# Kernel optimization log

Measured on AMD Instinct MI355X. Metric: run time of the kernel, lower is better.

## Reference

```python
import jax, jax.numpy as jnp
import numpy as np


def gcn_conv(x, src, dst, W, b, num_nodes):
    # PyG GCNConv with add_self_loops=True, symmetric normalization.
    # src/dst already include self-loops.
    ones = jnp.ones(src.shape[0], dtype=x.dtype)
    deg = jax.ops.segment_sum(ones, dst, num_segments=num_nodes)  # [N]
    dinv = jnp.where(deg > 0, jax.lax.rsqrt(deg), 0.0)
    norm = dinv[src] * dinv[dst]                                   # [E+N]
    h = x @ W                                                      # [N, out]
    msg = h[src] * norm[:, None]                                   # gather + scale
    out = jax.ops.segment_sum(msg, dst, num_segments=num_nodes)    # scatter-add
    return out + b


def setup_inputs() -> dict:
    key = jax.random.key(0)
    k1, k2, k3, k4 = jax.random.split(key, 4)
    N, E = 50000, 1600000
    IN, HID, OUT = 1536, 256, 128
    x = jax.random.normal(k1, (N, IN), dtype=jnp.float32)
    edge_index = jax.random.randint(k2, (2, E), 0, N, dtype=jnp.int64)
    # Glorot-style scaled weights
    W1 = jax.random.normal(k3, (IN, HID), dtype=jnp.float32) / np.sqrt(IN)
    W2 = jax.random.normal(k4, (HID, OUT), dtype=jnp.float32) / np.sqrt(HID)
    b1 = jnp.zeros((HID,), dtype=jnp.float32)
    b2 = jnp.zeros((OUT,), dtype=jnp.float32)
    return {"x": x, "edge_index": edge_index, "W1": W1, "b1": b1,
            "W2": W2, "b2": b2, "num_nodes": N}


def reference(x, edge_index, W1, b1, W2, b2, num_nodes):
    loop = jnp.arange(num_nodes, dtype=edge_index.dtype)
    src = jnp.concatenate([edge_index[0], loop])
    dst = jnp.concatenate([edge_index[1], loop])
    h = gcn_conv(x, src, dst, W1, b1, num_nodes)
    h = jax.nn.relu(h)
    h = gcn_conv(h, src, dst, W2, b2, num_nodes)
    # F.normalize(h, dim=1): x / max(||x||_2, 1e-12)
    nrm = jnp.linalg.norm(h, axis=1, keepdims=True)
    return h / jnp.maximum(nrm, 1e-12)
```

## Files before the change

kernel.cpp:

```cpp
#include <hip/hip_runtime.h>

typedef __attribute__((ext_vector_type(4))) float f32x4;
typedef __attribute__((ext_vector_type(2))) float f32x2;
typedef __attribute__((ext_vector_type(8))) short s16x8;
typedef __attribute__((ext_vector_type(4))) unsigned short u16x4;
typedef __attribute__((ext_vector_type(2))) unsigned short u16x2;

static __device__ __forceinline__ unsigned short f2bf(float f) {
  unsigned int u = __builtin_bit_cast(unsigned int, f);
  u += 0x7fffu + ((u >> 16) & 1u);
  return (unsigned short)(u >> 16);
}
static __device__ __forceinline__ float bf2f(unsigned short h) {
  unsigned int u = ((unsigned int)h) << 16;
  return __builtin_bit_cast(float, u);
}

__global__ void zero_k(int* p, int n) {
  int i = blockIdx.x * 256 + threadIdx.x;
  if (i < n) p[i] = 0;
}
__global__ void deg_count_k(const int* __restrict__ edges, int* cnt, int E) {
  int e = blockIdx.x * 256 + threadIdx.x;
  if (e < E) atomicAdd(&cnt[edges[E + e]], 1);
}
__global__ void dinv_k(const int* __restrict__ cnt, float* dinv, int N) {
  int i = blockIdx.x * 256 + threadIdx.x;
  if (i < N) dinv[i] = rsqrtf((float)(cnt[i] + 1));
}

__global__ __launch_bounds__(256) void scan1_k(const int* __restrict__ cnt,
                                               int* __restrict__ loc,
                                               int* __restrict__ bsum, int N) {
  int t = threadIdx.x;
  int i0 = blockIdx.x * 1024 + t * 4;
  int c[4];
#pragma unroll
  for (int j = 0; j < 4; ++j) c[j] = (i0 + j < N) ? cnt[i0 + j] : 0;
  int tsum = c[0] + c[1] + c[2] + c[3];
  int lane = t & 63, wv = t >> 6;
  int incl = tsum;
#pragma unroll
  for (int off = 1; off < 64; off <<= 1) {
    int u = __shfl_up(incl, off, 64);
    if (lane >= off) incl += u;
  }
  __shared__ int ws[4];
  if (lane == 63) ws[wv] = incl;
  __syncthreads();
  int wbase = 0;
  for (int w = 0; w < wv; ++w) wbase += ws[w];
  int run = wbase + incl - tsum;
#pragma unroll
  for (int j = 0; j < 4; ++j) {
    if (i0 + j < N) loc[i0 + j] = run;
    run += c[j];
  }
  if (t == 255) bsum[blockIdx.x] = wbase + incl;
}
__global__ void scan2_k(int* bsum, int nb) {
  int lane = threadIdx.x;
  int v = (lane < nb) ? bsum[lane] : 0;
  int incl = v;
#pragma unroll
  for (int off = 1; off < 64; off <<= 1) {
    int u = __shfl_up(incl, off, 64);
    if (lane >= off) incl += u;
  }
  if (lane < nb) bsum[lane] = incl - v;
}
__global__ void addoff_k(int* loc, const int* __restrict__ bsum, int N) {
  int i = blockIdx.x * 256 + threadIdx.x;
  if (i < N) loc[i] += bsum[i >> 10];
}
__global__ void fill_k(const int* __restrict__ edges, const int* __restrict__ row,
                       int* cursor, int* __restrict__ csr, int E) {
  int e = blockIdx.x * 256 + threadIdx.x;
  if (e < E) {
    int s = edges[e], d = edges[E + e];
    int pos = atomicAdd(&cursor[d], 1);
    csr[row[d] + pos] = s;
  }
}

__global__ void convw_k(const float* __restrict__ W, unsigned short* __restrict__ Wt, int K, int Nn) {
  int t = blockIdx.x * 256 + threadIdx.x;
  if (t < K * Nn) {
    int n = t / K;
    int k = t - n * K;
    Wt[n * K + k] = f2bf(W[(long long)k * Nn + n]);
  }
}

template <int KTOT, int NTOT, bool A_BF16>
__global__ __launch_bounds__(256, 2) void gemm_k(
    const void* __restrict__ Aptr, const unsigned short* __restrict__ Bt,
    const float* __restrict__ dinv, unsigned short* __restrict__ outg, int M) {
  constexpr int BM = 128, BK = 32, LD = BK + 8;
  constexpr int STRIP = NTOT / 4;
  constexpr int NF = STRIP / 16;
  constexpr int CH = NTOT / 64;

  __shared__ unsigned short Asm_[BM * LD];
  __shared__ unsigned short Bsm_[NTOT * LD];

  const int tid = threadIdx.x;
  const int wave = tid >> 6;
  const int lane = tid & 63;
  const int fr = lane & 15;
  const int quad = lane >> 4;
  const int m0 = blockIdx.x * BM;

  f32x4 acc[8][NF];
#pragma unroll
  for (int i = 0; i < 8; ++i)
#pragma unroll
    for (int j = 0; j < NF; ++j) { f32x4 z = {0.f, 0.f, 0.f, 0.f}; acc[i][j] = z; }

  const int sr = tid >> 1;
  const int sc = (tid & 1) << 4;
  const bool arow_ok = (m0 + sr) < M;
  const float* arowf = (const float*)Aptr + (long long)(m0 + sr) * KTOT;
  const unsigned short* arowh = (const unsigned short*)Aptr + (long long)(m0 + sr) * KTOT;

  float va[16];
  s16x8 vah[2];

  auto loadA = [&](int k0) {
    if constexpr (A_BF16) {
      if (arow_ok) {
        vah[0] = *(const s16x8*)(arowh + k0 + sc);
        vah[1] = *(const s16x8*)(arowh + k0 + sc + 8);
      } else {
        s16x8 z = {0, 0, 0, 0, 0, 0, 0, 0};
        vah[0] = z; vah[1] = z;
      }
    } else {
      if (arow_ok) {
        const f32x4* p = (const f32x4*)(arowf + k0 + sc);
        f32x4 v0 = p[0], v1 = p[1], v2 = p[2], v3 = p[3];
#pragma unroll
        for (int j = 0; j < 4; ++j) { va[j] = v0[j]; va[4 + j] = v1[j]; va[8 + j] = v2[j]; va[12 + j] = v3[j]; }
      } else {
#pragma unroll
        for (int j = 0; j < 16; ++j) va[j] = 0.0f;
      }
    }
  };
  s16x8 vb[CH];
  auto loadB = [&](int k0) {
#pragma unroll
    for (int c = 0; c < CH; ++c) {
      int ch = tid + c * 256;
      int br = ch >> 2;
      int bc = (ch & 3) << 3;
      vb[c] = *(const s16x8*)&Bt[(long long)br * KTOT + k0 + bc];
    }
  };

  loadA(0);
  loadB(0);

  for (int k0 = 0; k0 < KTOT; k0 += BK) {
    s16x8 h0, h1;
    if constexpr (A_BF16) {
      h0 = vah[0]; h1 = vah[1];
    } else {
#pragma unroll
      for (int j = 0; j < 8; ++j) { h0[j] = (short)f2bf(va[j]); h1[j] = (short)f2bf(va[8 + j]); }
    }
    s16x8 vbc[CH];
#pragma unroll
    for (int c = 0; c < CH; ++c) vbc[c] = vb[c];

    __syncthreads();
    *(s16x8*)&Asm_[sr * LD + sc] = h0;
    *(s16x8*)&Asm_[sr * LD + sc + 8] = h1;
#pragma unroll
    for (int c = 0; c < CH; ++c) {
      int ch = tid + c * 256;
      int br = ch >> 2;
      int bc = (ch & 3) << 3;
      *(s16x8*)&Bsm_[br * LD + bc] = vbc[c];
    }
    __syncthreads();

    if (k0 + BK < KTOT) { loadA(k0 + BK); loadB(k0 + BK); }

    s16x8 af[8], bfr[NF];
#pragma unroll
    for (int mi = 0; mi < 8; ++mi) af[mi] = *(const s16x8*)&Asm_[(mi * 16 + fr) * LD + quad * 8];
#pragma unroll
    for (int ni = 0; ni < NF; ++ni) bfr[ni] = *(const s16x8*)&Bsm_[(wave * STRIP + ni * 16 + fr) * LD + quad * 8];
#pragma unroll
    for (int mi = 0; mi < 8; ++mi)
#pragma unroll
      for (int ni = 0; ni < NF; ++ni)
        acc[mi][ni] = __builtin_amdgcn_mfma_f32_16x16x32_bf16(af[mi], bfr[ni], acc[mi][ni], 0, 0, 0);
  }

#pragma unroll
  for (int mi = 0; mi < 8; ++mi) {
    int mbase = mi * 16 + quad * 4;
#pragma unroll
    for (int r = 0; r < 4; ++r) {
      int gm = m0 + mbase + r;
      if (gm < M) {
        float dv = dinv[gm];
#pragma unroll
        for (int ni = 0; ni < NF; ++ni) {
          int col = wave * STRIP + ni * 16 + fr;
          outg[(long long)gm * NTOT + col] = f2bf(acc[mi][ni][r] * dv);
        }
      }
    }
  }
}

__global__ __launch_bounds__(256) void agg1_k(const int* __restrict__ csr,
                                              const int* __restrict__ row,
                                              const int* __restrict__ cnt,
                                              const unsigned short* __restrict__ g,
                                              const float* __restrict__ bias,
                                              const float* __restrict__ dinv,
                                              unsigned short* __restrict__ h, int N) {
  int node = blockIdx.x * 4 + (threadIdx.x >> 6);
  if (node >= N) return;
  int lane = threadIdx.x & 63;
  int f0 = lane << 2;
  u16x4 sv = *(const u16x4*)&g[(long long)node * 256 + f0];
  f32x4 s = {bf2f(sv[0]), bf2f(sv[1]), bf2f(sv[2]), bf2f(sv[3])};
  int start = row[node], len = cnt[node];
  int j = 0;
  for (; j + 8 <= len; j += 8) {
    int idx[8];
#pragma unroll
    for (int t = 0; t < 8; ++t) idx[t] = csr[start + j + t];
    u16x4 v[8];
#pragma unroll
    for (int t = 0; t < 8; ++t) v[t] = *(const u16x4*)&g[(long long)idx[t] * 256 + f0];
#pragma unroll
    for (int t = 0; t < 8; ++t) {
      s[0] += bf2f(v[t][0]); s[1] += bf2f(v[t][1]);
      s[2] += bf2f(v[t][2]); s[3] += bf2f(v[t][3]);
    }
  }
  for (; j < len; ++j) {
    int i0 = csr[start + j];
    u16x4 v = *(const u16x4*)&g[(long long)i0 * 256 + f0];
    s[0] += bf2f(v[0]); s[1] += bf2f(v[1]); s[2] += bf2f(v[2]); s[3] += bf2f(v[3]);
  }
  float dv = dinv[node];
  f32x4 b = *(const f32x4*)&bias[f0];
  u16x4 o;
#pragma unroll
  for (int k = 0; k < 4; ++k) o[k] = f2bf(fmaxf(0.0f, b[k] + dv * s[k]));
  *(u16x4*)&h[(long long)node * 256 + f0] = o;
}

__global__ __launch_bounds__(256) void agg2_k(const int* __restrict__ csr,
                                              const int* __restrict__ row,
                                              const int* __restrict__ cnt,
                                              const unsigned short* __restrict__ g,
                                              const float* __restrict__ b2,
                                              const float* __restrict__ dinv,
                                              float* __restrict__ out, int N) {
  int node = blockIdx.x * 4 + (threadIdx.x >> 6);
  if (node >= N) return;
  int lane = threadIdx.x & 63;
  int f0 = lane << 1;
  u16x2 sv = *(const u16x2*)&g[(long long)node * 128 + f0];
  float s0 = bf2f(sv[0]), s1 = bf2f(sv[1]);
  int start = row[node], len = cnt[node];
  int j = 0;
  for (; j + 8 <= len; j += 8) {
    int idx[8];
#pragma unroll
    for (int t = 0; t < 8; ++t) idx[t] = csr[start + j + t];
    u16x2 v[8];
#pragma unroll
    for (int t = 0; t < 8; ++t) v[t] = *(const u16x2*)&g[(long long)idx[t] * 128 + f0];
#pragma unroll
    for (int t = 0; t < 8; ++t) { s0 += bf2f(v[t][0]); s1 += bf2f(v[t][1]); }
  }
  for (; j < len; ++j) {
    int i0 = csr[start + j];
    u16x2 v = *(const u16x2*)&g[(long long)i0 * 128 + f0];
    s0 += bf2f(v[0]); s1 += bf2f(v[1]);
  }
  float dv = dinv[node];
  f32x2 b = *(const f32x2*)&b2[f0];
  float x0 = b[0] + dv * s0;
  float x1 = b[1] + dv * s1;
  float ss = x0 * x0 + x1 * x1;
#pragma unroll
  for (int off = 32; off > 0; off >>= 1) ss += __shfl_xor(ss, off, 64);
  float inv = 1.0f / fmaxf(sqrtf(ss), 1e-12f);
  f32x2 o = {x0 * inv, x1 * inv};
  *(f32x2*)&out[(long long)node * 128 + f0] = o;
}

extern "C" void kernel_launch(void* const* d_in, const int* in_sizes, int n_in,
                              void* d_out, int out_size, void* d_ws, size_t ws_size,
                              hipStream_t stream) {
  const float* x = (const float*)d_in[0];
  const int* edges = (const int*)d_in[1];
  const float* W1 = (const float*)d_in[2];
  const float* b1 = (const float*)d_in[3];
  const float* W2 = (const float*)d_in[4];
  const float* b2 = (const float*)d_in[5];
  float* out = (float*)d_out;

  const int HID = in_sizes[3];
  const int OUT = in_sizes[5];
  const int IN = in_sizes[2] / HID;
  const int N = in_sizes[0] / IN;
  const int E = in_sizes[1] / 2;

  size_t off = 0;
  auto carve = [&](size_t bytes) {
    void* p = (char*)d_ws + off;
    off += (bytes + 255) & ~(size_t)255;
    return p;
  };
  int* cnt = (int*)carve((size_t)N * 4);
  int* cursor = (int*)carve((size_t)N * 4);
  int* row = (int*)carve((size_t)N * 4);
  int* bsum = (int*)carve(64 * 4);
  int* csr = (int*)carve((size_t)E * 4);
  float* dinv = (float*)carve((size_t)N * 4);
  unsigned short* W1t = (unsigned short*)carve((size_t)IN * HID * 2);
  unsigned short* W2t = (unsigned short*)carve((size_t)HID * OUT * 2);
  unsigned short* g1 = (unsigned short*)carve((size_t)N * HID * 2);
  unsigned short* acc1 = (unsigned short*)carve((size_t)N * HID * 2);
  unsigned short* g2 = (unsigned short*)carve((size_t)N * OUT * 2);
  (void)ws_size; (void)n_in; (void)out_size;

  const int nb = (N + 1023) / 1024;

  zero_k<<<(N + 255) / 256, 256, 0, stream>>>(cnt, N);
  zero_k<<<(N + 255) / 256, 256, 0, stream>>>(cursor, N);
  deg_count_k<<<(E + 255) / 256, 256, 0, stream>>>(edges, cnt, E);
  dinv_k<<<(N + 255) / 256, 256, 0, stream>>>(cnt, dinv, N);

  scan1_k<<<nb, 256, 0, stream>>>(cnt, row, bsum, N);
  scan2_k<<<1, 64, 0, stream>>>(bsum, nb);
  addoff_k<<<(N + 255) / 256, 256, 0, stream>>>(row, bsum, N);
  fill_k<<<(E + 255) / 256, 256, 0, stream>>>(edges, row, cursor, csr, E);

  convw_k<<<(IN * HID + 255) / 256, 256, 0, stream>>>(W1, W1t, IN, HID);
  convw_k<<<(HID * OUT + 255) / 256, 256, 0, stream>>>(W2, W2t, HID, OUT);

  int mtiles = (N + 127) / 128;
  gemm_k<1536, 256, false><<<mtiles, 256, 0, stream>>>(x, W1t, dinv, g1, N);
  agg1_k<<<(N + 3) / 4, 256, 0, stream>>>(csr, row, cnt, g1, b1, dinv, acc1, N);
  gemm_k<256, 128, true><<<mtiles, 256, 0, stream>>>(acc1, W2t, dinv, g2, N);
  agg2_k<<<(N + 3) / 4, 256, 0, stream>>>(csr, row, cnt, g2, b2, dinv, out, N);
}
```

Baseline: 801.5 us.

## Slice features into 32-column tables, double-buffer GEMM with direct LDS loads

The GEMM now double-buffers LDS and stages B, plus A when it is bf16, through global_load_lds with an XOR swizzle. It writes its output in 32-column slice-major layout so that each aggregation pass gathers from a compact per-slice table that fits cache better. Aggregation is rewritten as a 2D grid over node groups and feature slices, with 8 lanes per node, masked loads and nontemporal accesses. The final L2 normalization is split into a separate kernel over an extra fp32 buffer, and the CSR fill now uses absolute cursors. The cost is more gather passes over the CSR index list, an extra intermediate buffer and launch, and divergence padding to the longest neighbour list within each wave.

```diff
diff --git a/kernel.cpp b/kernel.cpp
--- a/kernel.cpp
+++ b/kernel.cpp
@@ -4,7 +4,6 @@
 typedef __attribute__((ext_vector_type(2))) float f32x2;
 typedef __attribute__((ext_vector_type(8))) short s16x8;
 typedef __attribute__((ext_vector_type(4))) unsigned short u16x4;
-typedef __attribute__((ext_vector_type(2))) unsigned short u16x2;
 
 static __device__ __forceinline__ unsigned short f2bf(float f) {
   unsigned int u = __builtin_bit_cast(unsigned int, f);
@@ -14,6 +13,12 @@
 static __device__ __forceinline__ float bf2f(unsigned short h) {
   unsigned int u = ((unsigned int)h) << 16;
   return __builtin_bit_cast(float, u);
+}
+
+static __device__ __forceinline__ void gload_lds16(const void* g, void* l) {
+  __builtin_amdgcn_global_load_lds(
+      (const __attribute__((address_space(1))) unsigned int*)g,
+      (__attribute__((address_space(3))) unsigned int*)l, 16, 0, 0);
 }
 
 __global__ void zero_k(int* p, int n) {
@@ -69,17 +74,21 @@
   }
   if (lane < nb) bsum[lane] = incl - v;
 }
-__global__ void addoff_k(int* loc, const int* __restrict__ bsum, int N) {
+__global__ void addoff_k(int* loc, int* cursor, const int* __restrict__ bsum, int N) {
   int i = blockIdx.x * 256 + threadIdx.x;
-  if (i < N) loc[i] += bsum[i >> 10];
-}
-__global__ void fill_k(const int* __restrict__ edges, const int* __restrict__ row,
-                       int* cursor, int* __restrict__ csr, int E) {
+  if (i < N) {
+    int v = loc[i] + bsum[i >> 10];
+    loc[i] = v;
+    cursor[i] = v;
+  }
+}
+__global__ void fill_k(const int* __restrict__ edges, int* cursor,
+                       int* __restrict__ csr, int E) {
   int e = blockIdx.x * 256 + threadIdx.x;
   if (e < E) {
     int s = edges[e], d = edges[E + e];
     int pos = atomicAdd(&cursor[d], 1);
-    csr[row[d] + pos] = s;
+    csr[pos] = s;
   }
 }
 
@@ -96,13 +105,16 @@
 __global__ __launch_bounds__(256, 2) void gemm_k(
     const void* __restrict__ Aptr, const unsigned short* __restrict__ Bt,
     const float* __restrict__ dinv, unsigned short* __restrict__ outg, int M) {
-  constexpr int BM = 128, BK = 32, LD = BK + 8;
+  constexpr int BM = 128, BK = 32;
+  constexpr int LDA = BK + 8;
   constexpr int STRIP = NTOT / 4;
   constexpr int NF = STRIP / 16;
-  constexpr int CH = NTOT / 64;
-
-  __shared__ unsigned short Asm_[BM * LD];
-  __shared__ unsigned short Bsm_[NTOT * LD];
+  constexpr int BCH = (NTOT / 16) / 4;
+  constexpr int ACH = (BM / 16) / 4;
+  constexpr int NT = KTOT / BK;
+
+  __shared__ unsigned short Asm_[2][BM * LDA];
+  __shared__ unsigned short Bsm_[2][NTOT * BK];
 
   const int tid = threadIdx.x;
   const int wave = tid >> 6;
@@ -117,81 +129,87 @@
 #pragma unroll
     for (int j = 0; j < NF; ++j) { f32x4 z = {0.f, 0.f, 0.f, 0.f}; acc[i][j] = z; }
 
+  const int sl_r = lane >> 2;
+  const int sl_s = (lane & 3) ^ ((lane >> 3) & 3);
+
+  auto stageB = [&](int k0, int buf) {
+#pragma unroll
+    for (int c = 0; c < BCH; ++c) {
+      int cc = wave * BCH + c;
+      int r = cc * 16 + sl_r;
+      const unsigned short* gp = Bt + (long long)r * KTOT + k0 + sl_s * 8;
+      gload_lds16(gp, &Bsm_[buf][cc * 512]);
+    }
+  };
+  auto stageA_h = [&](int k0, int buf) {
+    const unsigned short* Ah = (const unsigned short*)Aptr;
+#pragma unroll
+    for (int c = 0; c < ACH; ++c) {
+      int cc = wave * ACH + c;
+      int r = cc * 16 + sl_r;
+      const unsigned short* gp = Ah + (long long)(m0 + r) * KTOT + k0 + sl_s * 8;
+      gload_lds16(gp, &Asm_[buf][cc * 512]);
+    }
+  };
+
   const int sr = tid >> 1;
   const int sc = (tid & 1) << 4;
   const bool arow_ok = (m0 + sr) < M;
   const float* arowf = (const float*)Aptr + (long long)(m0 + sr) * KTOT;
-  const unsigned short* arowh = (const unsigned short*)Aptr + (long long)(m0 + sr) * KTOT;
-
   float va[16];
-  s16x8 vah[2];
-
   auto loadA = [&](int k0) {
-    if constexpr (A_BF16) {
-      if (arow_ok) {
-        vah[0] = *(const s16x8*)(arowh + k0 + sc);
-        vah[1] = *(const s16x8*)(arowh + k0 + sc + 8);
+    if (arow_ok) {
+      const f32x4* p = (const f32x4*)(arowf + k0 + sc);
+      f32x4 v0 = p[0], v1 = p[1], v2 = p[2], v3 = p[3];
+#pragma unroll
+      for (int j = 0; j < 4; ++j) { va[j] = v0[j]; va[4 + j] = v1[j]; va[8 + j] = v2[j]; va[12 + j] = v3[j]; }
+    } else {
+#pragma unroll
+      for (int j = 0; j < 16; ++j) va[j] = 0.0f;
+    }
+  };
+  auto cvtWriteA = [&](int buf) {
+    s16x8 h0, h1;
+#pragma unroll
+    for (int j = 0; j < 8; ++j) { h0[j] = (short)f2bf(va[j]); h1[j] = (short)f2bf(va[8 + j]); }
+    *(s16x8*)&Asm_[buf][sr * LDA + sc] = h0;
+    *(s16x8*)&Asm_[buf][sr * LDA + sc + 8] = h1;
+  };
+
+  stageB(0, 0);
+  if constexpr (A_BF16) {
+    stageA_h(0, 0);
+  } else {
+    loadA(0);
+    cvtWriteA(0);
+    if (NT > 1) loadA(BK);
+  }
+
+  const int xsl = (fr >> 1) & 3;
+  for (int kt = 0; kt < NT; ++kt) {
+    const int cur = kt & 1;
+    __syncthreads();
+    if (kt + 1 < NT) {
+      stageB((kt + 1) * BK, cur ^ 1);
+      if constexpr (A_BF16) {
+        stageA_h((kt + 1) * BK, cur ^ 1);
       } else {
-        s16x8 z = {0, 0, 0, 0, 0, 0, 0, 0};
-        vah[0] = z; vah[1] = z;
+        cvtWriteA(cur ^ 1);
+        if (kt + 2 < NT) loadA((kt + 2) * BK);
       }
-    } else {
-      if (arow_ok) {
-        const f32x4* p = (const f32x4*)(arowf + k0 + sc);
-        f32x4 v0 = p[0], v1 = p[1], v2 = p[2], v3 = p[3];
-#pragma unroll
-        for (int j = 0; j < 4; ++j) { va[j] = v0[j]; va[4 + j] = v1[j]; va[8 + j] = v2[j]; va[12 + j] = v3[j]; }
-      } else {
-#pragma unroll
-        for (int j = 0; j < 16; ++j) va[j] = 0.0f;
-      }
-    }
-  };
-  s16x8 vb[CH];
-  auto loadB = [&](int k0) {
-#pragma unroll
-    for (int c = 0; c < CH; ++c) {
-      int ch = tid + c * 256;
-      int br = ch >> 2;
-      int bc = (ch & 3) << 3;
-      vb[c] = *(const s16x8*)&Bt[(long long)br * KTOT + k0 + bc];
-    }
-  };
-
-  loadA(0);
-  loadB(0);
-
-  for (int k0 = 0; k0 < KTOT; k0 += BK) {
-    s16x8 h0, h1;
-    if constexpr (A_BF16) {
-      h0 = vah[0]; h1 = vah[1];
-    } else {
-#pragma unroll
-      for (int j = 0; j < 8; ++j) { h0[j] = (short)f2bf(va[j]); h1[j] = (short)f2bf(va[8 + j]); }
-    }
-    s16x8 vbc[CH];
-#pragma unroll
-    for (int c = 0; c < CH; ++c) vbc[c] = vb[c];
-
-    __syncthreads();
-    *(s16x8*)&Asm_[sr * LD + sc] = h0;
-    *(s16x8*)&Asm_[sr * LD + sc + 8] = h1;
-#pragma unroll
-    for (int c = 0; c < CH; ++c) {
-      int ch = tid + c * 256;
-      int br = ch >> 2;
-      int bc = (ch & 3) << 3;
-      *(s16x8*)&Bsm_[br * LD + bc] = vbc[c];
-    }
-    __syncthreads();
-
-    if (k0 + BK < KTOT) { loadA(k0 + BK); loadB(k0 + BK); }
+    }
 
     s16x8 af[8], bfr[NF];
 #pragma unroll
-    for (int mi = 0; mi < 8; ++mi) af[mi] = *(const s16x8*)&Asm_[(mi * 16 + fr) * LD + quad * 8];
-#pragma unroll
-    for (int ni = 0; ni < NF; ++ni) bfr[ni] = *(const s16x8*)&Bsm_[(wave * STRIP + ni * 16 + fr) * LD + quad * 8];
+    for (int mi = 0; mi < 8; ++mi) {
+      if constexpr (A_BF16)
+        af[mi] = *(const s16x8*)&Asm_[cur][(mi * 16 + fr) * BK + ((quad ^ xsl) << 3)];
+      else
+        af[mi] = *(const s16x8*)&Asm_[cur][(mi * 16 + fr) * LDA + quad * 8];
+    }
+#pragma unroll
+    for (int ni = 0; ni < NF; ++ni)
+      bfr[ni] = *(const s16x8*)&Bsm_[cur][(wave * STRIP + ni * 16 + fr) * BK + ((quad ^ xsl) << 3)];
 #pragma unroll
     for (int mi = 0; mi < 8; ++mi)
 #pragma unroll
@@ -210,94 +228,90 @@
 #pragma unroll
         for (int ni = 0; ni < NF; ++ni) {
           int col = wave * STRIP + ni * 16 + fr;
-          outg[(long long)gm * NTOT + col] = f2bf(acc[mi][ni][r] * dv);
+          long long addr = ((long long)(col >> 5) * M + gm) * 32 + (col & 31);
+          outg[addr] = f2bf(acc[mi][ni][r] * dv);
         }
       }
     }
   }
 }
 
-__global__ __launch_bounds__(256) void agg1_k(const int* __restrict__ csr,
+template <int F, bool L1>
+__global__ __launch_bounds__(256) void aggs_k(const int* __restrict__ csr,
                                               const int* __restrict__ row,
                                               const int* __restrict__ cnt,
                                               const unsigned short* __restrict__ g,
                                               const float* __restrict__ bias,
                                               const float* __restrict__ dinv,
-                                              unsigned short* __restrict__ h, int N) {
-  int node = blockIdx.x * 4 + (threadIdx.x >> 6);
-  if (node >= N) return;
-  int lane = threadIdx.x & 63;
-  int f0 = lane << 2;
-  u16x4 sv = *(const u16x4*)&g[(long long)node * 256 + f0];
-  f32x4 s = {bf2f(sv[0]), bf2f(sv[1]), bf2f(sv[2]), bf2f(sv[3])};
-  int start = row[node], len = cnt[node];
-  int j = 0;
-  for (; j + 8 <= len; j += 8) {
-    int idx[8];
-#pragma unroll
-    for (int t = 0; t < 8; ++t) idx[t] = csr[start + j + t];
-    u16x4 v[8];
-#pragma unroll
-    for (int t = 0; t < 8; ++t) v[t] = *(const u16x4*)&g[(long long)idx[t] * 256 + f0];
-#pragma unroll
-    for (int t = 0; t < 8; ++t) {
-      s[0] += bf2f(v[t][0]); s[1] += bf2f(v[t][1]);
-      s[2] += bf2f(v[t][2]); s[3] += bf2f(v[t][3]);
-    }
-  }
-  for (; j < len; ++j) {
-    int i0 = csr[start + j];
-    u16x4 v = *(const u16x4*)&g[(long long)i0 * 256 + f0];
-    s[0] += bf2f(v[0]); s[1] += bf2f(v[1]); s[2] += bf2f(v[2]); s[3] += bf2f(v[3]);
-  }
-  float dv = dinv[node];
-  f32x4 b = *(const f32x4*)&bias[f0];
-  u16x4 o;
-#pragma unroll
-  for (int k = 0; k < 4; ++k) o[k] = f2bf(fmaxf(0.0f, b[k] + dv * s[k]));
-  *(u16x4*)&h[(long long)node * 256 + f0] = o;
-}
-
-__global__ __launch_bounds__(256) void agg2_k(const int* __restrict__ csr,
-                                              const int* __restrict__ row,
-                                              const int* __restrict__ cnt,
-                                              const unsigned short* __restrict__ g,
-                                              const float* __restrict__ b2,
-                                              const float* __restrict__ dinv,
+                                              void* __restrict__ outp, int N) {
+  const int wave = threadIdx.x >> 6, lane = threadIdx.x & 63;
+  const int grp = lane >> 3, sub = lane & 7;
+  const int node = blockIdx.x * 32 + wave * 8 + grp;
+  const bool ok = node < N;
+  const int nn = ok ? node : 0;
+  const int s = blockIdx.y;
+  const unsigned short* tbl = g + (long long)s * N * 32;
+  const int fo = sub * 4;
+
+  u16x4 sv = *(const u16x4*)&tbl[(long long)nn * 32 + fo];
+  f32x4 acc = {bf2f(sv[0]), bf2f(sv[1]), bf2f(sv[2]), bf2f(sv[3])};
+
+  int start = ok ? row[nn] : 0;
+  int len = ok ? cnt[nn] : 0;
+  int ml = len;
+  ml = max(ml, __shfl_xor(ml, 8, 64));
+  ml = max(ml, __shfl_xor(ml, 16, 64));
+  ml = max(ml, __shfl_xor(ml, 32, 64));
+
+  for (int j = 0; j < ml; j += 4) {
+    int idx[4];
+#pragma unroll
+    for (int t = 0; t < 4; ++t) {
+      int jt = j + t;
+      int p = start + ((jt < len) ? jt : 0);
+      int raw = __builtin_nontemporal_load(&csr[p]);
+      idx[t] = (jt < len) ? raw : 0;
+    }
+    u16x4 v[4];
+#pragma unroll
+    for (int t = 0; t < 4; ++t) v[t] = *(const u16x4*)&tbl[(long long)idx[t] * 32 + fo];
+#pragma unroll
+    for (int t = 0; t < 4; ++t) {
+      float m = ((j + t) < len) ? 1.0f : 0.0f;
+#pragma unroll
+      for (int k = 0; k < 4; ++k) acc[k] += m * bf2f(v[t][k]);
+    }
+  }
+
+  if (ok) {
+    float dv = dinv[node];
+    f32x4 b = *(const f32x4*)&bias[s * 32 + fo];
+    if constexpr (L1) {
+      u16x4 o;
+#pragma unroll
+      for (int k = 0; k < 4; ++k) o[k] = f2bf(fmaxf(0.0f, b[k] + dv * acc[k]));
+      __builtin_nontemporal_store(o, (u16x4*)&((unsigned short*)outp)[(long long)node * F + s * 32 + fo]);
+    } else {
+      f32x4 o;
+#pragma unroll
+      for (int k = 0; k < 4; ++k) o[k] = b[k] + dv * acc[k];
+      __builtin_nontemporal_store(o, (f32x4*)&((float*)outp)[(long long)node * F + s * 32 + fo]);
+    }
+  }
+}
+
+__global__ __launch_bounds__(256) void norm_k(const float* __restrict__ pre,
                                               float* __restrict__ out, int N) {
   int node = blockIdx.x * 4 + (threadIdx.x >> 6);
   if (node >= N) return;
   int lane = threadIdx.x & 63;
-  int f0 = lane << 1;
-  u16x2 sv = *(const u16x2*)&g[(long long)node * 128 + f0];
-  float s0 = bf2f(sv[0]), s1 = bf2f(sv[1]);
-  int start = row[node], len = cnt[node];
-  int j = 0;
-  for (; j + 8 <= len; j += 8) {
-    int idx[8];
-#pragma unroll
-    for (int t = 0; t < 8; ++t) idx[t] = csr[start + j + t];
-    u16x2 v[8];
-#pragma unroll
-    for (int t = 0; t < 8; ++t) v[t] = *(const u16x2*)&g[(long long)idx[t] * 128 + f0];
-#pragma unroll
-    for (int t = 0; t < 8; ++t) { s0 += bf2f(v[t][0]); s1 += bf2f(v[t][1]); }
-  }
-  for (; j < len; ++j) {
-    int i0 = csr[start + j];
-    u16x2 v = *(const u16x2*)&g[(long long)i0 * 128 + f0];
-    s0 += bf2f(v[0]); s1 += bf2f(v[1]);
-  }
-  float dv = dinv[node];
-  f32x2 b = *(const f32x2*)&b2[f0];
-  float x0 = b[0] + dv * s0;
-  float x1 = b[1] + dv * s1;
-  float ss = x0 * x0 + x1 * x1;
+  f32x2 v = *(const f32x2*)&pre[(long long)node * 128 + lane * 2];
+  float ss = v[0] * v[0] + v[1] * v[1];
 #pragma unroll
   for (int off = 32; off > 0; off >>= 1) ss += __shfl_xor(ss, off, 64);
   float inv = 1.0f / fmaxf(sqrtf(ss), 1e-12f);
-  f32x2 o = {x0 * inv, x1 * inv};
-  *(f32x2*)&out[(long long)node * 128 + f0] = o;
+  f32x2 o = {v[0] * inv, v[1] * inv};
+  *(f32x2*)&out[(long long)node * 128 + lane * 2] = o;
 }
 
 extern "C" void kernel_launch(void* const* d_in, const int* in_sizes, int n_in,
@@ -327,33 +341,35 @@
   int* cursor = (int*)carve((size_t)N * 4);
   int* row = (int*)carve((size_t)N * 4);
   int* bsum = (int*)carve(64 * 4);
-  int* csr = (int*)carve((size_t)E * 4);
+  int* csr = (int*)carve((size_t)E * 4 + 1024);
   float* dinv = (float*)carve((size_t)N * 4);
   unsigned short* W1t = (unsigned short*)carve((size_t)IN * HID * 2);
   unsigned short* W2t = (unsigned short*)carve((size_t)HID * OUT * 2);
   unsigned short* g1 = (unsigned short*)carve((size_t)N * HID * 2);
   unsigned short* acc1 = (unsigned short*)carve((size_t)N * HID * 2);
   unsigned short* g2 = (unsigned short*)carve((size_t)N * OUT * 2);
+  float* pre = (float*)carve((size_t)N * OUT * 4);
   (void)ws_size; (void)n_in; (void)out_size;
 
   const int nb = (N + 1023) / 1024;
 
   zero_k<<<(N + 255) / 256, 256, 0, stream>>>(cnt, N);
-  zero_k<<<(N + 255) / 256, 256, 0, stream>>>(cursor, N);
   deg_count_k<<<(E + 255) / 256, 256, 0, stream>>>(edges, cnt, E);
   dinv_k<<<(N + 255) / 256, 256, 0, stream>>>(cnt, dinv, N);
 
   scan1_k<<<nb, 256, 0, stream>>>(cnt, row, bsum, N);
   scan2_k<<<1, 64, 0, stream>>>(bsum, nb);
-  addoff_k<<<(N + 255) / 256, 256, 0, stream>>>(row, bsum, N);
-  fill_k<<<(E + 255) / 256, 256, 0, stream>>>(edges, row, cursor, csr, E);
+  addoff_k<<<(N + 255) / 256, 256, 0, stream>>>(row, cursor, bsum, N);
+  fill_k<<<(E + 255) / 256, 256, 0, stream>>>(edges, cursor, csr, E);
 
   convw_k<<<(IN * HID + 255) / 256, 256, 0, stream>>>(W1, W1t, IN, HID);
   convw_k<<<(HID * OUT + 255) / 256, 256, 0, stream>>>(W2, W2t, HID, OUT);
 
   int mtiles = (N + 127) / 128;
+  int nb32 = (N + 31) / 32;
   gemm_k<1536, 256, false><<<mtiles, 256, 0, stream>>>(x, W1t, dinv, g1, N);
-  agg1_k<<<(N + 3) / 4, 256, 0, stream>>>(csr, row, cnt, g1, b1, dinv, acc1, N);
+  aggs_k<256, true><<<dim3(nb32, 8), 256, 0, stream>>>(csr, row, cnt, g1, b1, dinv, acc1, N);
   gemm_k<256, 128, true><<<mtiles, 256, 0, stream>>>(acc1, W2t, dinv, g2, N);
-  agg2_k<<<(N + 3) / 4, 256, 0, stream>>>(csr, row, cnt, g2, b2, dinv, out, N);
-}
+  aggs_k<128, false><<<dim3(nb32, 4), 256, 0, stream>>>(csr, row, cnt, g2, b2, dinv, pre, N);
+  norm_k<<<(N + 3) / 4, 256, 0, stream>>>(pre, out, N);
+}
```

New measurement: 1.038 ms. 1.3x slower.
